# Kernel tuning notes

Hardware: AMD Instinct MI355X
Metric: run time of the kernel (lower is better)

## Reference

```python
import jax, jax.numpy as jnp
import numpy as np

NH, NKV, D = 16, 4, 64
E, NG, TKG, TOPK = 64, 8, 4, 8
RSF = 2.5
EPS = 1e-6
THETA = 10000.0

def rmsnorm(x, w, eps=EPS):
    v = jnp.mean(jnp.square(x.astype(jnp.float32)), axis=-1, keepdims=True)
    return (x * jax.lax.rsqrt(v + eps)).astype(x.dtype) * w

def rope_neox(x, pos):
    # x: [T, heads, D]; neox-style rotation over full head_dim
    d = x.shape[-1]
    inv = 1.0 / (THETA ** (jnp.arange(0, d, 2, dtype=jnp.float32) / d))
    f = pos.astype(jnp.float32)[:, None] * inv              # [T, d/2]
    cos = jnp.cos(f)[:, None, :]
    sin = jnp.sin(f)[:, None, :]
    x1, x2 = jnp.split(x, 2, axis=-1)
    return jnp.concatenate([x1 * cos - x2 * sin, x2 * cos + x1 * sin], axis=-1)


def setup_inputs() -> dict:
    key = jax.random.key(0)
    ks = jax.random.split(key, 12)
    T, H, I, IS = 2048, 1024, 256, 512
    s = 0.02
    return {
        "x": jax.random.normal(ks[0], (T, H), jnp.float32),
        "positions": jnp.arange(T, dtype=jnp.int32),
        "ln1_w": jnp.ones((H,), jnp.float32),
        "w_qkv": jax.random.normal(ks[1], (H, (NH + 2 * NKV) * D), jnp.float32) * s,
        "w_o": jax.random.normal(ks[2], (NH * D, H), jnp.float32) * s,
        "ln2_w": jnp.ones((H,), jnp.float32),
        "gate_w": jax.random.normal(ks[3], (E, H), jnp.float32) * s,
        "expert_bias": jax.random.normal(ks[4], (E,), jnp.float32) * 0.01,
        "we_gate": jax.random.normal(ks[5], (E, H, I), jnp.float32) * s,
        "we_up": jax.random.normal(ks[6], (E, H, I), jnp.float32) * s,
        "we_down": jax.random.normal(ks[7], (E, I, H), jnp.float32) * s,
        "ws_gate_up": jax.random.normal(ks[8], (H, 2 * IS), jnp.float32) * s,
        "ws_down": jax.random.normal(ks[9], (IS, H), jnp.float32) * s,
    }


def reference(x, positions, ln1_w, w_qkv, w_o, ln2_w, gate_w, expert_bias,
              we_gate, we_up, we_down, ws_gate_up, ws_down):
    T, H = x.shape
    residual = x
    # --- attention ---
    h = rmsnorm(x, ln1_w)
    qkv = h @ w_qkv
    q, k, v = jnp.split(qkv, [NH * D, (NH + NKV) * D], axis=-1)
    q = rope_neox(q.reshape(T, NH, D), positions)
    k = rope_neox(k.reshape(T, NKV, D), positions)
    v = v.reshape(T, NKV, D)
    rep = NH // NKV
    k = jnp.repeat(k, rep, axis=1)
    v = jnp.repeat(v, rep, axis=1)
    scores = jnp.einsum('thd,shd->hts', q, k) * (D ** -0.5)
    causal = positions[:, None] >= positions[None, :]
    scores = jnp.where(causal[None], scores, jnp.float32(-1e30))
    p = jax.nn.softmax(scores, axis=-1)
    attn = jnp.einsum('hts,shd->thd', p, v).reshape(T, NH * D)
    residual = residual + attn @ w_o
    # --- MoE block ---
    h = rmsnorm(residual, ln2_w)
    logits = h.astype(jnp.float32) @ gate_w.astype(jnp.float32).T      # [T,E]
    s = jax.nn.sigmoid(logits)
    sc = s + expert_bias[None, :]                                      # bias-corrected scores
    # grouped top-k: score each group by sum of its top-2 corrected scores
    gsc = sc.reshape(T, NG, E // NG)
    group_scores = jax.lax.top_k(gsc, 2)[0].sum(-1)                    # [T,NG]
    _, gidx = jax.lax.top_k(group_scores, TKG)
    gmask = jnp.zeros((T, NG), bool).at[jnp.arange(T)[:, None], gidx].set(True)
    sc_masked = jnp.where(jnp.repeat(gmask, E // NG, axis=1), sc, -jnp.inf)
    _, ids = jax.lax.top_k(sc_masked, TOPK)                            # [T,k]
    w = jnp.take_along_axis(s, ids, axis=-1)                           # weights from raw sigmoid scores
    w = w / (w.sum(-1, keepdims=True) + 1e-20)
    w = w * RSF
    combine = jnp.zeros((T, E), jnp.float32).at[jnp.arange(T)[:, None], ids].add(w)
    combine = combine.astype(h.dtype)
    # routed experts (dense-over-experts reference of the grouped-GEMM dispatch)
    g = jnp.einsum('th,ehi->tei', h, we_gate)
    u = jnp.einsum('th,ehi->tei', h, we_up)
    act = jax.nn.silu(g) * u
    y = jnp.einsum('tei,eih,te->th', act, we_down, combine)
    # shared expert (SwiGLU)
    gu = h @ ws_gate_up
    gs, us = jnp.split(gu, 2, axis=-1)
    y = y + (jax.nn.silu(gs) * us) @ ws_down
    return residual + y
```

## Files before the change

kernel.cpp:

```cpp
#include <hip/hip_runtime.h>
#include <hip/hip_bf16.h>
#include <math.h>

#define T_TOK 2048
#define H_DIM 1024
#define NHH 16
#define NKVH 4
#define HD 64
#define QKV_N 1536
#define NE 64
#define NGRP 8
#define TKG 4
#define TOPKK 8
#define EI 256
#define ISH 512
#define NPOS (T_TOK * TOPKK)

typedef __bf16 bf16_t;
typedef bf16_t bf16x8 __attribute__((ext_vector_type(8)));
typedef bf16_t bf16x4v __attribute__((ext_vector_type(4)));
typedef float f32x4 __attribute__((ext_vector_type(4)));

#define MFMA_BF16 __builtin_amdgcn_mfma_f32_16x16x32_bf16

#define GLOAD16(gsrc, ldst)                                            \
  __builtin_amdgcn_global_load_lds(                                    \
      (const __attribute__((address_space(1))) void*)(gsrc),           \
      (__attribute__((address_space(3))) void*)(ldst), 16, 0, 0)

__global__ void rmsnorm_k(const float* __restrict__ x, const float* __restrict__ w,
                          float* __restrict__ outf, bf16_t* __restrict__ outb) {
  const int t = blockIdx.x;
  const int tid = threadIdx.x;
  const float* xp = x + (size_t)t * H_DIM;
  const float4 x4 = *(const float4*)(xp + tid * 4);
  float s = x4.x * x4.x + x4.y * x4.y + x4.z * x4.z + x4.w * x4.w;
#pragma unroll
  for (int off = 32; off >= 1; off >>= 1) s += __shfl_xor(s, off);
  __shared__ float red[4];
  if ((tid & 63) == 0) red[tid >> 6] = s;
  __syncthreads();
  const float tot = red[0] + red[1] + red[2] + red[3];
  const float r = rsqrtf(tot / (float)H_DIM + 1e-6f);
  const float4 w4 = *(const float4*)(w + tid * 4);
  float4 o;
  o.x = x4.x * r * w4.x; o.y = x4.y * r * w4.y;
  o.z = x4.z * r * w4.z; o.w = x4.w * r * w4.w;
  if (outf) *(float4*)(outf + (size_t)t * H_DIM + tid * 4) = o;
  bf16x4v ob;
  ob[0] = (bf16_t)o.x; ob[1] = (bf16_t)o.y; ob[2] = (bf16_t)o.z; ob[3] = (bf16_t)o.w;
  *(bf16x4v*)(outb + (size_t)t * H_DIM + tid * 4) = ob;
}

__global__ void castT_k(const float* __restrict__ src, bf16_t* __restrict__ dst,
                        int R, int C, size_t srcStride, size_t dstStride,
                        int dstLD, int rowOff) {
  const int e = blockIdx.z;
  const float* sp = src + (size_t)e * srcStride;
  bf16_t* dp = dst + (size_t)e * dstStride;
  const int r0 = blockIdx.y * 32, c0 = blockIdx.x * 32;
  const int tid = threadIdx.x;
  __shared__ float tl[32][33];
  {
    const int rr = tid >> 3, cc4 = (tid & 7) * 4;
    const float4 v = *(const float4*)(sp + (size_t)(r0 + rr) * C + c0 + cc4);
    tl[rr][cc4 + 0] = v.x; tl[rr][cc4 + 1] = v.y;
    tl[rr][cc4 + 2] = v.z; tl[rr][cc4 + 3] = v.w;
  }
  __syncthreads();
  {
    const int cc = tid >> 3, rr4 = (tid & 7) * 4;
    bf16x4v o;
#pragma unroll
    for (int i = 0; i < 4; i++) o[i] = (bf16_t)tl[rr4 + i][cc];
    *(bf16x4v*)(dp + (size_t)(rowOff + c0 + cc) * dstLD + r0 + rr4) = o;
  }
}


__global__ __launch_bounds__(256) void mfma_gemm_k(
    const bf16_t* __restrict__ A, const bf16_t* __restrict__ Bt,
    const float* __restrict__ add0, const float* __restrict__ add1,
    float* __restrict__ C, int M, int N, int K) {
  __shared__ bf16_t Al[128 * 64];
  __shared__ bf16_t Bl[128 * 64];
  const int tid = threadIdx.x;
  const int lane = tid & 63, wave = tid >> 6;
  const int wm = wave >> 1, wn = wave & 1;
  const int lrow = lane & 15, lq = lane >> 4;
  const int m0 = blockIdx.y * 128, n0 = blockIdx.x * 128;
  f32x4 acc[4][4];
#pragma unroll
  for (int i = 0; i < 4; i++)
#pragma unroll
    for (int j = 0; j < 4; j++) acc[i][j] = (f32x4){0.f, 0.f, 0.f, 0.f};
  for (int k0 = 0; k0 < K; k0 += 64) {
    __syncthreads();
#pragma unroll
    for (int i = 0; i < 4; i++) {
      const int j = wave * 4 + i;
      const int rowl = j * 8 + (lane >> 3);
      const int q = (lane & 7) ^ ((rowl >> 1) & 7);
      GLOAD16(A + (size_t)(m0 + rowl) * K + k0 + q * 8, &Al[j * 512]);
      GLOAD16(Bt + (size_t)(n0 + rowl) * K + k0 + q * 8, &Bl[j * 512]);
    }
    __syncthreads();
#pragma unroll
    for (int kb = 0; kb < 2; kb++) {
      const int qq = kb * 4 + lq;
      bf16x8 af[4], bfr[4];
#pragma unroll
      for (int i = 0; i < 4; i++) {
        const int ra = wm * 64 + i * 16 + lrow;
        const int rb = wn * 64 + i * 16 + lrow;
        af[i]  = *(const bf16x8*)&Al[(ra * 8 + (qq ^ ((ra >> 1) & 7))) * 8];
        bfr[i] = *(const bf16x8*)&Bl[(rb * 8 + (qq ^ ((rb >> 1) & 7))) * 8];
      }
#pragma unroll
      for (int i = 0; i < 4; i++)
#pragma unroll
        for (int j = 0; j < 4; j++)
          acc[i][j] = MFMA_BF16(af[i], bfr[j], acc[i][j], 0, 0, 0);
    }
  }
#pragma unroll
  for (int i = 0; i < 4; i++)
#pragma unroll
    for (int r = 0; r < 4; r++) {
      const int m = m0 + wm * 64 + i * 16 + lq * 4 + r;
#pragma unroll
      for (int j = 0; j < 4; j++) {
        const int n = n0 + wn * 64 + j * 16 + lrow;
        float v = acc[i][j][r];
        if (add0) v += add0[(size_t)m * N + n];
        if (add1) v += add1[(size_t)m * N + n];
        C[(size_t)m * N + n] = v;
      }
    }
}

__global__ __launch_bounds__(256) void mfma_gateup_k(
    const bf16_t* __restrict__ h2b, const bf16_t* __restrict__ weT,
    const int* __restrict__ ptok, const int* __restrict__ offs,
    bf16_t* __restrict__ gu_e) {
  const int e = blockIdx.z;
  const int base = offs[e];
  const int cnt = offs[e + 1] - base;
  const int m0 = blockIdx.y * 128;
  if (m0 >= cnt) return;
  const int n0 = blockIdx.x * 128;
  __shared__ bf16_t Al[128 * 64];
  __shared__ bf16_t Bl[128 * 64];
  __shared__ int toks[128];
  const int tid = threadIdx.x;
  if (tid < 128) toks[tid] = ptok[base + min(m0 + tid, cnt - 1)];
  const int lane = tid & 63, wave = tid >> 6;
  const int wm = wave >> 1, wn = wave & 1;
  const int lrow = lane & 15, lq = lane >> 4;
  const bf16_t* Bt = weT + (size_t)e * 512 * 1024 + (size_t)n0 * 1024;
  f32x4 acc[4][4];
#pragma unroll
  for (int i = 0; i < 4; i++)
#pragma unroll
    for (int j = 0; j < 4; j++) acc[i][j] = (f32x4){0.f, 0.f, 0.f, 0.f};
  for (int k0 = 0; k0 < 1024; k0 += 64) {
    __syncthreads();
#pragma unroll
    for (int i = 0; i < 4; i++) {
      const int j = wave * 4 + i;
      const int rowl = j * 8 + (lane >> 3);
      const int q = (lane & 7) ^ ((rowl >> 1) & 7);
      GLOAD16(h2b + (size_t)toks[rowl] * 1024 + k0 + q * 8, &Al[j * 512]);
      GLOAD16(Bt + (size_t)rowl * 1024 + k0 + q * 8, &Bl[j * 512]);
    }
    __syncthreads();
#pragma unroll
    for (int kb = 0; kb < 2; kb++) {
      const int qq = kb * 4 + lq;
      bf16x8 af[4], bfr[4];
#pragma unroll
      for (int i = 0; i < 4; i++) {
        const int ra = wm * 64 + i * 16 + lrow;
        const int rb = wn * 64 + i * 16 + lrow;
        af[i]  = *(const bf16x8*)&Al[(ra * 8 + (qq ^ ((ra >> 1) & 7))) * 8];
        bfr[i] = *(const bf16x8*)&Bl[(rb * 8 + (qq ^ ((rb >> 1) & 7))) * 8];
      }
#pragma unroll
      for (int i = 0; i < 4; i++)
#pragma unroll
        for (int j = 0; j < 4; j++)
          acc[i][j] = MFMA_BF16(af[i], bfr[j], acc[i][j], 0, 0, 0);
    }
  }
#pragma unroll
  for (int i = 0; i < 4; i++)
#pragma unroll
    for (int r = 0; r < 4; r++) {
      const int mloc = m0 + wm * 64 + i * 16 + lq * 4 + r;
      if (mloc < cnt) {
#pragma unroll
        for (int j = 0; j < 4; j++) {
          const int n = n0 + wn * 64 + j * 16 + lrow;
          gu_e[(size_t)(base + mloc) * 512 + n] = (bf16_t)acc[i][j][r];
        }
      }
    }
}

__global__ __launch_bounds__(256) void mfma_down_k(
    const bf16_t* __restrict__ actb, const bf16_t* __restrict__ wdT,
    const int* __restrict__ ptok, const float* __restrict__ pw,
    const int* __restrict__ offs, float* __restrict__ y) {
  const int e = blockIdx.z;
  const int base = offs[e];
  const int cnt = offs[e + 1] - base;
  const int m0 = blockIdx.y * 128;
  if (m0 >= cnt) return;
  const int n0 = blockIdx.x * 128;
  __shared__ bf16_t Al[128 * 64];
  __shared__ bf16_t Bl[128 * 64];
  const int tid = threadIdx.x;
  const int lane = tid & 63, wave = tid >> 6;
  const int wm = wave >> 1, wn = wave & 1;
  const int lrow = lane & 15, lq = lane >> 4;
  const bf16_t* Bt = wdT + (size_t)e * 1024 * 256 + (size_t)n0 * 256;
  f32x4 acc[4][4];
#pragma unroll
  for (int i = 0; i < 4; i++)
#pragma unroll
    for (int j = 0; j < 4; j++) acc[i][j] = (f32x4){0.f, 0.f, 0.f, 0.f};
  for (int k0 = 0; k0 < 256; k0 += 64) {
    __syncthreads();
#pragma unroll
    for (int i = 0; i < 4; i++) {
      const int j = wave * 4 + i;
      const int rowl = j * 8 + (lane >> 3);
      const int q = (lane & 7) ^ ((rowl >> 1) & 7);
      const int aRow = base + min(m0 + rowl, cnt - 1);
      GLOAD16(actb + (size_t)aRow * 256 + k0 + q * 8, &Al[j * 512]);
      GLOAD16(Bt + (size_t)rowl * 256 + k0 + q * 8, &Bl[j * 512]);
    }
    __syncthreads();
#pragma unroll
    for (int kb = 0; kb < 2; kb++) {
      const int qq = kb * 4 + lq;
      bf16x8 af[4], bfr[4];
#pragma unroll
      for (int i = 0; i < 4; i++) {
        const int ra = wm * 64 + i * 16 + lrow;
        const int rb = wn * 64 + i * 16 + lrow;
        af[i]  = *(const bf16x8*)&Al[(ra * 8 + (qq ^ ((ra >> 1) & 7))) * 8];
        bfr[i] = *(const bf16x8*)&Bl[(rb * 8 + (qq ^ ((rb >> 1) & 7))) * 8];
      }
#pragma unroll
      for (int i = 0; i < 4; i++)
#pragma unroll
        for (int j = 0; j < 4; j++)
          acc[i][j] = MFMA_BF16(af[i], bfr[j], acc[i][j], 0, 0, 0);
    }
  }
#pragma unroll
  for (int i = 0; i < 4; i++)
#pragma unroll
    for (int r = 0; r < 4; r++) {
      const int mloc = m0 + wm * 64 + i * 16 + lq * 4 + r;
      if (mloc < cnt) {
        const float wv = pw[base + mloc];
        const int tok = ptok[base + mloc];
#pragma unroll
        for (int j = 0; j < 4; j++) {
          const int n = n0 + wn * 64 + j * 16 + lrow;
          atomicAdd(&y[(size_t)tok * H_DIM + n], wv * acc[i][j][r]);
        }
      }
    }
}

__global__ void rope_k(float* __restrict__ qkv, const int* __restrict__ positions) {
  const int t = blockIdx.x, h = blockIdx.y;
  const int i = threadIdx.x;
  const float inv = exp2f((float)i * (-13.287712379549449f / 32.0f));
  const float f = (float)positions[t] * inv;
  float sn, c;
  sincosf(f, &sn, &c);
  float* p = qkv + (size_t)t * QKV_N + h * HD;
  const float x1 = p[i], x2 = p[i + 32];
  p[i] = x1 * c - x2 * sn;
  p[i + 32] = x2 * c + x1 * sn;
}

__global__ __launch_bounds__(256) void kvprep_k(
    const float* __restrict__ qkv, bf16_t* __restrict__ kh, bf16_t* __restrict__ kl,
    bf16_t* __restrict__ vh, bf16_t* __restrict__ vl) {
  const int tile = blockIdx.x, g = blockIdx.y;
  const int tid = threadIdx.x;
  const int srow = tid >> 2, scb = tid & 3;
  const int t = tile * 64 + srow;
  const float* kp = qkv + (size_t)t * QKV_N + NHH * HD + g * HD + scb * 16;
  const float* vp = kp + NKVH * HD;
  __shared__ bf16_t Vsh[64][72];
  __shared__ bf16_t Vsl[64][72];
  {
    const float4 k0 = *(const float4*)(kp + 0);
    const float4 k1 = *(const float4*)(kp + 4);
    const float4 k2 = *(const float4*)(kp + 8);
    const float4 k3 = *(const float4*)(kp + 12);
    const float kv[16] = {k0.x, k0.y, k0.z, k0.w, k1.x, k1.y, k1.z, k1.w,
                          k2.x, k2.y, k2.z, k2.w, k3.x, k3.y, k3.z, k3.w};
    bf16x8 h0, h1, o0, o1;
#pragma unroll
    for (int j = 0; j < 8; j++) {
      const bf16_t hi = (bf16_t)kv[j];
      h0[j] = hi; o0[j] = (bf16_t)(kv[j] - (float)hi);
      const bf16_t hi2 = (bf16_t)kv[j + 8];
      h1[j] = hi2; o1[j] = (bf16_t)(kv[j + 8] - (float)hi2);
    }
    bf16_t* khp = kh + ((size_t)g * T_TOK + t) * 64 + scb * 16;
    bf16_t* klp = kl + ((size_t)g * T_TOK + t) * 64 + scb * 16;
    *(bf16x8*)(khp) = h0; *(bf16x8*)(khp + 8) = h1;
    *(bf16x8*)(klp) = o0; *(bf16x8*)(klp + 8) = o1;
  }
  {
    const float4 v0 = *(const float4*)(vp + 0);
    const float4 v1 = *(const float4*)(vp + 4);
    const float4 v2 = *(const float4*)(vp + 8);
    const float4 v3 = *(const float4*)(vp + 12);
    const float vv[16] = {v0.x, v0.y, v0.z, v0.w, v1.x, v1.y, v1.z, v1.w,
                          v2.x, v2.y, v2.z, v2.w, v3.x, v3.y, v3.z, v3.w};
#pragma unroll
    for (int r2 = 0; r2 < 16; r2++) {
      const int d = scb * 16 + r2;
      const int col = (srow + (d & 56)) & 63;
      const bf16_t hi = (bf16_t)vv[r2];
      Vsh[d][col] = hi;
      Vsl[d][col] = (bf16_t)(vv[r2] - (float)hi);
    }
  }
  __syncthreads();
  {
    const size_t ob = (((size_t)g * (T_TOK / 64) + tile) * 64 + srow) * 64 + scb * 16;
    *(bf16x8*)(vh + ob)     = *(const bf16x8*)&Vsh[srow][scb * 16];
    *(bf16x8*)(vh + ob + 8) = *(const bf16x8*)&Vsh[srow][scb * 16 + 8];
    *(bf16x8*)(vl + ob)     = *(const bf16x8*)&Vsl[srow][scb * 16];
    *(bf16x8*)(vl + ob + 8) = *(const bf16x8*)&Vsl[srow][scb * 16 + 8];
  }
}

__global__ __launch_bounds__(256) void attn_k(
    const float* __restrict__ qkv, const bf16_t* __restrict__ kh_g,
    const bf16_t* __restrict__ kl_g, const bf16_t* __restrict__ vh_g,
    const bf16_t* __restrict__ vl_g, bf16_t* __restrict__ attnb) {
  const int h = blockIdx.x;
  const int qt = (T_TOK / 64 - 1) - blockIdx.y;
  const int g = h >> 2;
  const int tid = threadIdx.x;
  const int lane = tid & 63, wave = tid >> 6;
  const int lcol = lane & 15, lk = lane >> 4;

  __shared__ bf16_t Kh[64][72];
  __shared__ bf16_t Ko[64][72];
  __shared__ bf16_t Vh[64][72];
  __shared__ bf16_t Vl[64][72];
  __shared__ bf16_t Ph[64][72];
  __shared__ bf16_t Po[64][72];

  bf16x8 aqh[2], aql[2];
  {
    const int qrow = qt * 64 + wave * 16 + lcol;
    const float* qp = qkv + (size_t)qrow * QKV_N + h * HD + lk * 8;
#pragma unroll
    for (int ks = 0; ks < 2; ks++) {
      const float4 a = *(const float4*)(qp + ks * 32);
      const float4 b = *(const float4*)(qp + ks * 32 + 4);
      const float qv[8] = {a.x, a.y, a.z, a.w, b.x, b.y, b.z, b.w};
#pragma unroll
      for (int j = 0; j < 8; j++) {
        const float v = qv[j] * 0.125f;
        const bf16_t hi = (bf16_t)v;
        aqh[ks][j] = hi;
        aql[ks][j] = (bf16_t)(v - (float)hi);
      }
    }
  }

  float m[4], l[4];
  f32x4 acc[4];
#pragma unroll
  for (int r = 0; r < 4; r++) { m[r] = -1e30f; l[r] = 0.f; }
#pragma unroll
  for (int n = 0; n < 4; n++) acc[n] = (f32x4){0.f, 0.f, 0.f, 0.f};

  const bf16_t* khB = kh_g + (size_t)g * T_TOK * 64;
  const bf16_t* klB = kl_g + (size_t)g * T_TOK * 64;
  const bf16_t* vhB = vh_g + (size_t)g * (T_TOK / 64) * 64 * 64;
  const bf16_t* vlB = vl_g + (size_t)g * (T_TOK / 64) * 64 * 64;
  const int srow = tid >> 2;
  const int scb = tid & 3;

  for (int s0 = 0; s0 <= qt * 64; s0 += 64) {
    __syncthreads();
    {
      const size_t kb0 = (size_t)(s0 + srow) * 64 + scb * 16;
      *(bf16x8*)&Kh[srow][scb * 16]     = *(const bf16x8*)(khB + kb0);
      *(bf16x8*)&Kh[srow][scb * 16 + 8] = *(const bf16x8*)(khB + kb0 + 8);
      *(bf16x8*)&Ko[srow][scb * 16]     = *(const bf16x8*)(klB + kb0);
      *(bf16x8*)&Ko[srow][scb * 16 + 8] = *(const bf16x8*)(klB + kb0 + 8);
      const size_t vb0 = ((size_t)(s0 >> 6) * 64 + srow) * 64 + scb * 16;
      *(bf16x8*)&Vh[srow][scb * 16]     = *(const bf16x8*)(vhB + vb0);
      *(bf16x8*)&Vh[srow][scb * 16 + 8] = *(const bf16x8*)(vhB + vb0 + 8);
      *(bf16x8*)&Vl[srow][scb * 16]     = *(const bf16x8*)(vlB + vb0);
      *(bf16x8*)&Vl[srow][scb * 16 + 8] = *(const bf16x8*)(vlB + vb0 + 8);
    }
    __syncthreads();
    f32x4 s4[4];
#pragma unroll
    for (int n = 0; n < 4; n++) s4[n] = (f32x4){0.f, 0.f, 0.f, 0.f};
#pragma unroll
    for (int ks = 0; ks < 2; ks++) {
#pragma unroll
      for (int n = 0; n < 4; n++) {
        const bf16x8 bh = *(const bf16x8*)&Kh[n * 16 + lcol][ks * 32 + lk * 8];
        const bf16x8 bo = *(const bf16x8*)&Ko[n * 16 + lcol][ks * 32 + lk * 8];
        s4[n] = MFMA_BF16(aqh[ks], bh, s4[n], 0, 0, 0);
        s4[n] = MFMA_BF16(aqh[ks], bo, s4[n], 0, 0, 0);
        s4[n] = MFMA_BF16(aql[ks], bh, s4[n], 0, 0, 0);
      }
    }
    if (s0 == qt * 64) {
#pragma unroll
      for (int n = 0; n < 4; n++) {
        const int col = n * 16 + lcol;
#pragma unroll
        for (int r = 0; r < 4; r++)
          if (col > wave * 16 + lk * 4 + r) s4[n][r] = -1e30f;
      }
    }
#pragma unroll
    for (int r = 0; r < 4; r++) {
      float mx = fmaxf(fmaxf(s4[0][r], s4[1][r]), fmaxf(s4[2][r], s4[3][r]));
#pragma unroll
      for (int off = 1; off <= 8; off <<= 1) mx = fmaxf(mx, __shfl_xor(mx, off));
      const float mnew = fmaxf(m[r], mx);
      const float alpha = expf(m[r] - mnew);
      float ps = 0.f;
#pragma unroll
      for (int n = 0; n < 4; n++) {
        const float p = expf(s4[n][r] - mnew);
        s4[n][r] = p; ps += p;
      }
#pragma unroll
      for (int off = 1; off <= 8; off <<= 1) ps += __shfl_xor(ps, off);
      l[r] = l[r] * alpha + ps;
      m[r] = mnew;
#pragma unroll
      for (int n = 0; n < 4; n++) acc[n][r] *= alpha;
    }
#pragma unroll
    for (int n = 0; n < 4; n++)
#pragma unroll
      for (int r = 0; r < 4; r++) {
        const float p = s4[n][r];
        const bf16_t hi = (bf16_t)p;
        Ph[wave * 16 + lk * 4 + r][n * 16 + lcol] = hi;
        Po[wave * 16 + lk * 4 + r][n * 16 + lcol] = (bf16_t)(p - (float)hi);
      }
    __syncthreads();
#pragma unroll
    for (int ks = 0; ks < 2; ks++) {
      const bf16x8 pah = *(const bf16x8*)&Ph[wave * 16 + lcol][ks * 32 + lk * 8];
      const bf16x8 pao = *(const bf16x8*)&Po[wave * 16 + lcol][ks * 32 + lk * 8];
#pragma unroll
      for (int n = 0; n < 4; n++) {
        const int d = n * 16 + lcol;
        const int c0 = (ks * 32 + lk * 8 + (d & 56)) & 63;
        const bf16x8 bvh = *(const bf16x8*)&Vh[d][c0];
        const bf16x8 bvl = *(const bf16x8*)&Vl[d][c0];
        acc[n] = MFMA_BF16(pah, bvh, acc[n], 0, 0, 0);
        acc[n] = MFMA_BF16(pah, bvl, acc[n], 0, 0, 0);
        acc[n] = MFMA_BF16(pao, bvh, acc[n], 0, 0, 0);
      }
    }
  }
#pragma unroll
  for (int r = 0; r < 4; r++) {
    const int trow = qt * 64 + wave * 16 + lk * 4 + r;
    const float invl = 1.f / l[r];
#pragma unroll
    for (int n = 0; n < 4; n++)
      attnb[(size_t)trow * (NHH * HD) + h * HD + n * 16 + lcol] =
          (bf16_t)(acc[n][r] * invl);
  }
}

__global__ void gate_logits_k(const float* __restrict__ h2, const float* __restrict__ gw,
                              float* __restrict__ logits) {
  const int t = blockIdx.x;
  const int e = threadIdx.x;
  const float* hp = h2 + (size_t)t * H_DIM;
  const float* gp = gw + (size_t)e * H_DIM;
  float s = 0.f;
  for (int i = 0; i < H_DIM; i += 4) {
    const float4 h4 = *(const float4*)(hp + i);
    const float4 g4 = *(const float4*)(gp + i);
    s += h4.x * g4.x + h4.y * g4.y + h4.z * g4.z + h4.w * g4.w;
  }
  logits[t * NE + e] = s;
}

__global__ void route_k(const float* __restrict__ logits, const float* __restrict__ ebias,
                        int* __restrict__ topk_ids, float* __restrict__ topk_w) {
  const int t = blockIdx.x * 64 + threadIdx.x;
  if (t >= T_TOK) return;
  float s[NE], sc[NE];
  const float* lp = logits + t * NE;
#pragma unroll
  for (int e = 0; e < NE; e++) {
    const float v = 1.f / (1.f + expf(-lp[e]));
    s[e] = v;
    sc[e] = v + ebias[e];
  }
  float gsc[NGRP];
#pragma unroll
  for (int gi = 0; gi < NGRP; gi++) {
    float m1 = -1e30f, m2 = -1e30f;
#pragma unroll
    for (int j = 0; j < 8; j++) {
      const float v = sc[gi * 8 + j];
      if (v > m1) { m2 = m1; m1 = v; } else if (v > m2) m2 = v;
    }
    gsc[gi] = m1 + m2;
  }
  unsigned gmask = 0;
  for (int k2 = 0; k2 < TKG; k2++) {
    int bi = 0; float b = -3.4e38f;
#pragma unroll
    for (int gi = 0; gi < NGRP; gi++)
      if (!((gmask >> gi) & 1u) && gsc[gi] > b) { b = gsc[gi]; bi = gi; }
    gmask |= 1u << bi;
  }
  unsigned long long esel = 0ull;
  float wsum = 0.f;
  int ids[TOPKK]; float wv[TOPKK];
  for (int k2 = 0; k2 < TOPKK; k2++) {
    int bi = 0; float b = -3.4e38f;
    for (int e = 0; e < NE; e++) {
      if (((gmask >> (e >> 3)) & 1u) && !((esel >> e) & 1ull) && sc[e] > b) { b = sc[e]; bi = e; }
    }
    esel |= 1ull << bi;
    ids[k2] = bi;
    wv[k2] = s[bi];
    wsum += wv[k2];
  }
  const float norm = 2.5f / (wsum + 1e-20f);
#pragma unroll
  for (int k2 = 0; k2 < TOPKK; k2++) {
    topk_ids[t * TOPKK + k2] = ids[k2];
    topk_w[t * TOPKK + k2] = wv[k2] * norm;
  }
}

__global__ void count_k(const int* __restrict__ ids, int* __restrict__ counts) {
  const int idx = blockIdx.x * 256 + threadIdx.x;
  if (idx < NPOS) atomicAdd(&counts[ids[idx]], 1);
}

__global__ void offsets_k(const int* __restrict__ counts, int* __restrict__ offsets,
                          int* __restrict__ cursor) {
  if (threadIdx.x == 0 && blockIdx.x == 0) {
    int acc = 0;
    for (int e = 0; e < NE; e++) { offsets[e] = acc; cursor[e] = acc; acc += counts[e]; }
    offsets[NE] = acc;
  }
}

__global__ void scatter_k(const int* __restrict__ ids, const float* __restrict__ wts,
                          int* __restrict__ cursor, int* __restrict__ perm_tok,
                          float* __restrict__ perm_w) {
  const int idx = blockIdx.x * 256 + threadIdx.x;
  if (idx >= NPOS) return;
  const int e = ids[idx];
  const int pos = atomicAdd(&cursor[e], 1);
  perm_tok[pos] = idx >> 3;
  perm_w[pos] = wts[idx];
}

__global__ void act2_k(const bf16_t* __restrict__ gu_e, bf16_t* __restrict__ actb) {
  const int row = blockIdx.x;
  const int c = threadIdx.x;
  const float g = (float)gu_e[(size_t)row * 512 + c];
  const float u = (float)gu_e[(size_t)row * 512 + 256 + c];
  actb[(size_t)row * 256 + c] = (bf16_t)(g / (1.f + expf(-g)) * u);
}

__global__ void sact_k(const float* __restrict__ gu, bf16_t* __restrict__ sa) {
  const int idx = blockIdx.x * 256 + threadIdx.x;
  const int t = idx >> 9, i = idx & 511;
  const float g = gu[(size_t)t * 1024 + i];
  const float u = gu[(size_t)t * 1024 + 512 + i];
  sa[idx] = (bf16_t)(g / (1.f + expf(-g)) * u);
}

extern "C" void kernel_launch(void* const* d_in, const int* in_sizes, int n_in,
                              void* d_out, int out_size, void* d_ws, size_t ws_size,
                              hipStream_t stream) {
  const float* x         = (const float*)d_in[0];
  const int*   positions = (const int*)d_in[1];
  const float* ln1_w     = (const float*)d_in[2];
  const float* w_qkv     = (const float*)d_in[3];
  const float* w_o       = (const float*)d_in[4];
  const float* ln2_w     = (const float*)d_in[5];
  const float* gate_w    = (const float*)d_in[6];
  const float* ebias     = (const float*)d_in[7];
  const float* we_gate   = (const float*)d_in[8];
  const float* we_up     = (const float*)d_in[9];
  const float* we_down   = (const float*)d_in[10];
  const float* ws_gateup = (const float*)d_in[11];
  const float* ws_down   = (const float*)d_in[12];
  float* out = (float*)d_out;

  char* wsp = (char*)d_ws;
  size_t off = 0;
  auto alloc = [&](size_t bytes) {
    void* p = wsp + off;
    off += (bytes + 255) & ~(size_t)255;
    return p;
  };
  float*  qkv    = (float*)alloc((size_t)T_TOK * QKV_N * 4);
  bf16_t* attnb  = (bf16_t*)alloc((size_t)T_TOK * H_DIM * 2);
  bf16_t* gu_e   = (bf16_t*)qkv;
  bf16_t* h1b    = (bf16_t*)alloc((size_t)T_TOK * H_DIM * 2);
  bf16_t* sa     = h1b;
  float*  resid1 = (float*)alloc((size_t)T_TOK * H_DIM * 4);
  float*  h2f    = (float*)alloc((size_t)T_TOK * H_DIM * 4);
  bf16_t* h2b    = (bf16_t*)alloc((size_t)T_TOK * H_DIM * 2);
  float*  logits = (float*)alloc((size_t)T_TOK * NE * 4);
  int*    tids   = (int*)alloc((size_t)NPOS * 4);
  float*  tw     = (float*)alloc((size_t)NPOS * 4);
  int*    counts = (int*)alloc(NE * 4);
  int*    offs   = (int*)alloc((NE + 1) * 4);
  int*    cursor = (int*)alloc(NE * 4);
  int*    ptok   = (int*)alloc((size_t)NPOS * 4);
  float*  pw     = (float*)alloc((size_t)NPOS * 4);
  bf16_t* actb   = (bf16_t*)alloc((size_t)NPOS * EI * 2);
  float*  y      = (float*)alloc((size_t)T_TOK * H_DIM * 4);
  float*  gu     = (float*)alloc((size_t)T_TOK * 1024 * 4);
  bf16_t* wqkvT  = (bf16_t*)alloc((size_t)QKV_N * H_DIM * 2);
  bf16_t* woT    = (bf16_t*)alloc((size_t)H_DIM * H_DIM * 2);
  bf16_t* wsguT  = (bf16_t*)alloc((size_t)1024 * H_DIM * 2);
  bf16_t* wsdT   = (bf16_t*)alloc((size_t)H_DIM * ISH * 2);
  bf16_t* weT    = (bf16_t*)alloc((size_t)NE * 512 * H_DIM * 2);
  bf16_t* wdT    = (bf16_t*)alloc((size_t)NE * H_DIM * EI * 2);
  bf16_t* kvkh   = (bf16_t*)alloc((size_t)NKVH * T_TOK * 64 * 2);
  bf16_t* kvkl   = (bf16_t*)alloc((size_t)NKVH * T_TOK * 64 * 2);
  bf16_t* kvvh   = (bf16_t*)alloc((size_t)NKVH * T_TOK * 64 * 2);
  bf16_t* kvvl   = (bf16_t*)alloc((size_t)NKVH * T_TOK * 64 * 2);
  (void)ws_size; (void)in_sizes; (void)n_in; (void)out_size;

  castT_k<<<dim3(QKV_N / 32, H_DIM / 32, 1), 256, 0, stream>>>(
      w_qkv, wqkvT, H_DIM, QKV_N, 0, 0, H_DIM, 0);
  castT_k<<<dim3(H_DIM / 32, H_DIM / 32, 1), 256, 0, stream>>>(
      w_o, woT, H_DIM, H_DIM, 0, 0, H_DIM, 0);
  castT_k<<<dim3(1024 / 32, H_DIM / 32, 1), 256, 0, stream>>>(
      ws_gateup, wsguT, H_DIM, 1024, 0, 0, H_DIM, 0);
  castT_k<<<dim3(H_DIM / 32, ISH / 32, 1), 256, 0, stream>>>(
      ws_down, wsdT, ISH, H_DIM, 0, 0, ISH, 0);
  castT_k<<<dim3(EI / 32, H_DIM / 32, NE), 256, 0, stream>>>(
      we_gate, weT, H_DIM, EI, (size_t)H_DIM * EI, (size_t)512 * H_DIM, H_DIM, 0);
  castT_k<<<dim3(EI / 32, H_DIM / 32, NE), 256, 0, stream>>>(
      we_up, weT, H_DIM, EI, (size_t)H_DIM * EI, (size_t)512 * H_DIM, H_DIM, 256);
  castT_k<<<dim3(H_DIM / 32, EI / 32, NE), 256, 0, stream>>>(
      we_down, wdT, EI, H_DIM, (size_t)EI * H_DIM, (size_t)H_DIM * EI, EI, 0);

  hipMemsetAsync(counts, 0, NE * 4, stream);
  hipMemsetAsync(y, 0, (size_t)T_TOK * H_DIM * 4, stream);

  rmsnorm_k<<<T_TOK, 256, 0, stream>>>(x, ln1_w, nullptr, h1b);
  mfma_gemm_k<<<dim3(QKV_N / 128, T_TOK / 128), 256, 0, stream>>>(
      h1b, wqkvT, nullptr, nullptr, qkv, T_TOK, QKV_N, H_DIM);
  rope_k<<<dim3(T_TOK, NHH + NKVH), 32, 0, stream>>>(qkv, positions);
  kvprep_k<<<dim3(T_TOK / 64, NKVH), 256, 0, stream>>>(qkv, kvkh, kvkl, kvvh, kvvl);
  attn_k<<<dim3(NHH, T_TOK / 64), 256, 0, stream>>>(qkv, kvkh, kvkl, kvvh, kvvl, attnb);
  mfma_gemm_k<<<dim3(H_DIM / 128, T_TOK / 128), 256, 0, stream>>>(
      attnb, woT, x, nullptr, resid1, T_TOK, H_DIM, H_DIM);

  rmsnorm_k<<<T_TOK, 256, 0, stream>>>(resid1, ln2_w, h2f, h2b);
  gate_logits_k<<<T_TOK, 64, 0, stream>>>(h2f, gate_w, logits);
  route_k<<<T_TOK / 64, 64, 0, stream>>>(logits, ebias, tids, tw);
  count_k<<<NPOS / 256, 256, 0, stream>>>(tids, counts);
  offsets_k<<<1, 1, 0, stream>>>(counts, offs, cursor);
  scatter_k<<<NPOS / 256, 256, 0, stream>>>(tids, tw, cursor, ptok, pw);

  mfma_gateup_k<<<dim3(512 / 128, T_TOK / 128, NE), 256, 0, stream>>>(
      h2b, weT, ptok, offs, gu_e);
  act2_k<<<NPOS, 256, 0, stream>>>(gu_e, actb);
  mfma_down_k<<<dim3(H_DIM / 128, T_TOK / 128, NE), 256, 0, stream>>>(
      actb, wdT, ptok, pw, offs, y);

  mfma_gemm_k<<<dim3(1024 / 128, T_TOK / 128), 256, 0, stream>>>(
      h2b, wsguT, nullptr, nullptr, gu, T_TOK, 1024, H_DIM);
  sact_k<<<(T_TOK * ISH) / 256, 256, 0, stream>>>(gu, sa);
  mfma_gemm_k<<<dim3(H_DIM / 128, T_TOK / 128), 256, 0, stream>>>(
      sa, wsdT, resid1, y, out, T_TOK, H_DIM, ISH);
}
```

Measured before the change: 816.2 us.

## Double-buffer LDS tiles in MFMA GEMM kernels to overlap loads with compute

```diff
diff --git a/kernel.cpp b/kernel.cpp
--- a/kernel.cpp
+++ b/kernel.cpp
@@ -82,8 +82,8 @@
     const bf16_t* __restrict__ A, const bf16_t* __restrict__ Bt,
     const float* __restrict__ add0, const float* __restrict__ add1,
     float* __restrict__ C, int M, int N, int K) {
-  __shared__ bf16_t Al[128 * 64];
-  __shared__ bf16_t Bl[128 * 64];
+  __shared__ bf16_t Al[2][128 * 64];
+  __shared__ bf16_t Bl[2][128 * 64];
   const int tid = threadIdx.x;
   const int lane = tid & 63, wave = tid >> 6;
   const int wm = wave >> 1, wn = wave & 1;
@@ -94,17 +94,18 @@
   for (int i = 0; i < 4; i++)
 #pragma unroll
     for (int j = 0; j < 4; j++) acc[i][j] = (f32x4){0.f, 0.f, 0.f, 0.f};
-  for (int k0 = 0; k0 < K; k0 += 64) {
-    __syncthreads();
+
+  auto stage = [&](int b, int k0) {
 #pragma unroll
     for (int i = 0; i < 4; i++) {
       const int j = wave * 4 + i;
       const int rowl = j * 8 + (lane >> 3);
       const int q = (lane & 7) ^ ((rowl >> 1) & 7);
-      GLOAD16(A + (size_t)(m0 + rowl) * K + k0 + q * 8, &Al[j * 512]);
-      GLOAD16(Bt + (size_t)(n0 + rowl) * K + k0 + q * 8, &Bl[j * 512]);
-    }
-    __syncthreads();
+      GLOAD16(A + (size_t)(m0 + rowl) * K + k0 + q * 8, &Al[b][j * 512]);
+      GLOAD16(Bt + (size_t)(n0 + rowl) * K + k0 + q * 8, &Bl[b][j * 512]);
+    }
+  };
+  auto compute = [&](int b) {
 #pragma unroll
     for (int kb = 0; kb < 2; kb++) {
       const int qq = kb * 4 + lq;
@@ -113,8 +114,8 @@
       for (int i = 0; i < 4; i++) {
         const int ra = wm * 64 + i * 16 + lrow;
         const int rb = wn * 64 + i * 16 + lrow;
-        af[i]  = *(const bf16x8*)&Al[(ra * 8 + (qq ^ ((ra >> 1) & 7))) * 8];
-        bfr[i] = *(const bf16x8*)&Bl[(rb * 8 + (qq ^ ((rb >> 1) & 7))) * 8];
+        af[i]  = *(const bf16x8*)&Al[b][(ra * 8 + (qq ^ ((ra >> 1) & 7))) * 8];
+        bfr[i] = *(const bf16x8*)&Bl[b][(rb * 8 + (qq ^ ((rb >> 1) & 7))) * 8];
       }
 #pragma unroll
       for (int i = 0; i < 4; i++)
@@ -122,7 +123,19 @@
         for (int j = 0; j < 4; j++)
           acc[i][j] = MFMA_BF16(af[i], bfr[j], acc[i][j], 0, 0, 0);
     }
-  }
+  };
+
+  stage(0, 0);
+  __syncthreads();
+  int cur = 0;
+  for (int k0 = 64; k0 < K; k0 += 64) {
+    stage(cur ^ 1, k0);
+    compute(cur);
+    __syncthreads();
+    cur ^= 1;
+  }
+  compute(cur);
+
 #pragma unroll
   for (int i = 0; i < 4; i++)
 #pragma unroll
@@ -149,8 +162,8 @@
   const int m0 = blockIdx.y * 128;
   if (m0 >= cnt) return;
   const int n0 = blockIdx.x * 128;
-  __shared__ bf16_t Al[128 * 64];
-  __shared__ bf16_t Bl[128 * 64];
+  __shared__ bf16_t Al[2][128 * 64];
+  __shared__ bf16_t Bl[2][128 * 64];
   __shared__ int toks[128];
   const int tid = threadIdx.x;
   if (tid < 128) toks[tid] = ptok[base + min(m0 + tid, cnt - 1)];
@@ -163,17 +176,18 @@
   for (int i = 0; i < 4; i++)
 #pragma unroll
     for (int j = 0; j < 4; j++) acc[i][j] = (f32x4){0.f, 0.f, 0.f, 0.f};
-  for (int k0 = 0; k0 < 1024; k0 += 64) {
-    __syncthreads();
+
+  auto stage = [&](int b, int k0) {
 #pragma unroll
     for (int i = 0; i < 4; i++) {
       const int j = wave * 4 + i;
       const int rowl = j * 8 + (lane >> 3);
       const int q = (lane & 7) ^ ((rowl >> 1) & 7);
-      GLOAD16(h2b + (size_t)toks[rowl] * 1024 + k0 + q * 8, &Al[j * 512]);
-      GLOAD16(Bt + (size_t)rowl * 1024 + k0 + q * 8, &Bl[j * 512]);
-    }
-    __syncthreads();
+      GLOAD16(h2b + (size_t)toks[rowl] * 1024 + k0 + q * 8, &Al[b][j * 512]);
+      GLOAD16(Bt + (size_t)rowl * 1024 + k0 + q * 8, &Bl[b][j * 512]);
+    }
+  };
+  auto compute = [&](int b) {
 #pragma unroll
     for (int kb = 0; kb < 2; kb++) {
       const int qq = kb * 4 + lq;
@@ -182,8 +196,8 @@
       for (int i = 0; i < 4; i++) {
         const int ra = wm * 64 + i * 16 + lrow;
         const int rb = wn * 64 + i * 16 + lrow;
-        af[i]  = *(const bf16x8*)&Al[(ra * 8 + (qq ^ ((ra >> 1) & 7))) * 8];
-        bfr[i] = *(const bf16x8*)&Bl[(rb * 8 + (qq ^ ((rb >> 1) & 7))) * 8];
+        af[i]  = *(const bf16x8*)&Al[b][(ra * 8 + (qq ^ ((ra >> 1) & 7))) * 8];
+        bfr[i] = *(const bf16x8*)&Bl[b][(rb * 8 + (qq ^ ((rb >> 1) & 7))) * 8];
       }
 #pragma unroll
       for (int i = 0; i < 4; i++)
@@ -191,7 +205,20 @@
         for (int j = 0; j < 4; j++)
           acc[i][j] = MFMA_BF16(af[i], bfr[j], acc[i][j], 0, 0, 0);
     }
-  }
+  };
+
+  __syncthreads();
+  stage(0, 0);
+  __syncthreads();
+  int cur = 0;
+  for (int k0 = 64; k0 < 1024; k0 += 64) {
+    stage(cur ^ 1, k0);
+    compute(cur);
+    __syncthreads();
+    cur ^= 1;
+  }
+  compute(cur);
+
 #pragma unroll
   for (int i = 0; i < 4; i++)
 #pragma unroll
@@ -217,8 +244,8 @@
   const int m0 = blockIdx.y * 128;
   if (m0 >= cnt) return;
   const int n0 = blockIdx.x * 128;
-  __shared__ bf16_t Al[128 * 64];
-  __shared__ bf16_t Bl[128 * 64];
+  __shared__ bf16_t Al[2][128 * 64];
+  __shared__ bf16_t Bl[2][128 * 64];
   const int tid = threadIdx.x;
   const int lane = tid & 63, wave = tid >> 6;
   const int wm = wave >> 1, wn = wave & 1;
@@ -229,18 +256,19 @@
   for (int i = 0; i < 4; i++)
 #pragma unroll
     for (int j = 0; j < 4; j++) acc[i][j] = (f32x4){0.f, 0.f, 0.f, 0.f};
-  for (int k0 = 0; k0 < 256; k0 += 64) {
-    __syncthreads();
+
+  auto stage = [&](int b, int k0) {
 #pragma unroll
     for (int i = 0; i < 4; i++) {
       const int j = wave * 4 + i;
       const int rowl = j * 8 + (lane >> 3);
       const int q = (lane & 7) ^ ((rowl >> 1) & 7);
       const int aRow = base + min(m0 + rowl, cnt - 1);
-      GLOAD16(actb + (size_t)aRow * 256 + k0 + q * 8, &Al[j * 512]);
-      GLOAD16(Bt + (size_t)rowl * 256 + k0 + q * 8, &Bl[j * 512]);
-    }
-    __syncthreads();
+      GLOAD16(actb + (size_t)aRow * 256 + k0 + q * 8, &Al[b][j * 512]);
+      GLOAD16(Bt + (size_t)rowl * 256 + k0 + q * 8, &Bl[b][j * 512]);
+    }
+  };
+  auto compute = [&](int b) {
 #pragma unroll
     for (int kb = 0; kb < 2; kb++) {
       const int qq = kb * 4 + lq;
@@ -249,8 +277,8 @@
       for (int i = 0; i < 4; i++) {
         const int ra = wm * 64 + i * 16 + lrow;
         const int rb = wn * 64 + i * 16 + lrow;
-        af[i]  = *(const bf16x8*)&Al[(ra * 8 + (qq ^ ((ra >> 1) & 7))) * 8];
-        bfr[i] = *(const bf16x8*)&Bl[(rb * 8 + (qq ^ ((rb >> 1) & 7))) * 8];
+        af[i]  = *(const bf16x8*)&Al[b][(ra * 8 + (qq ^ ((ra >> 1) & 7))) * 8];
+        bfr[i] = *(const bf16x8*)&Bl[b][(rb * 8 + (qq ^ ((rb >> 1) & 7))) * 8];
       }
 #pragma unroll
       for (int i = 0; i < 4; i++)
@@ -258,7 +286,19 @@
         for (int j = 0; j < 4; j++)
           acc[i][j] = MFMA_BF16(af[i], bfr[j], acc[i][j], 0, 0, 0);
     }
-  }
+  };
+
+  stage(0, 0);
+  __syncthreads();
+  int cur = 0;
+  for (int k0 = 64; k0 < 256; k0 += 64) {
+    stage(cur ^ 1, k0);
+    compute(cur);
+    __syncthreads();
+    cur ^= 1;
+  }
+  compute(cur);
+
 #pragma unroll
   for (int i = 0; i < 4; i++)
 #pragma unroll
```

After: 846.2 us. +3.7%, slower.
